# Performance work log

Measured on AMD Instinct MI355X. Metric: run time of the kernel, lower is better.

Reference implementation:

```python
import jax, jax.numpy as jnp
import numpy as np

B, T, D = 4, 2048, 1024


def setup_inputs() -> dict:
    key = jax.random.key(0)
    ks = jax.random.split(key, 7)
    s = 1.0 / np.sqrt(D)
    return {
        "x": jax.random.normal(ks[0], (B, T, D), dtype=jnp.float32),
        "Wq": jax.random.normal(ks[1], (D, D), dtype=jnp.float32) * s,
        "bq": jax.random.normal(ks[2], (D,), dtype=jnp.float32) * s,
        "Wk": jax.random.normal(ks[3], (D, D), dtype=jnp.float32) * s,
        "bk": jax.random.normal(ks[4], (D,), dtype=jnp.float32) * s,
        "Wv": jax.random.normal(ks[5], (D, D), dtype=jnp.float32) * s,
        "bv": jax.random.normal(ks[6], (D,), dtype=jnp.float32) * s,
    }


def reference(x, Wq, bq, Wk, bk, Wv, bv):
    # Linear projections (torch nn.Linear: y = x @ W.T + b)
    Q = jnp.einsum('btd,ed->bte', x, Wq) + bq  # computed for faithfulness; unused downstream
    K = jnp.einsum('btd,ed->bte', x, Wk) + bk
    V = jnp.einsum('btd,ed->bte', x, Wv) + bv
    # Quantum kernel closed form: <ZZ> of RY(a)q0, RY(b)q1, CX(0,1) == cos(b).
    # score[b,i,j] = cos(mean_d K[b,j,d]) -- independent of i (and of Q).
    kmean = K.mean(axis=-1)                      # [B, T]
    scores = jnp.cos(kmean)[:, None, :]          # [B, 1, T] -> broadcast over i
    scores = jax.lax.stop_gradient(jnp.broadcast_to(scores, (Q.shape[0], Q.shape[1], Q.shape[1])))
    weights = jax.nn.softmax(scores, axis=-1)    # [B, T, T]
    return jnp.einsum('bij,bjd->bid', weights, V)
```

## Files before the change

### kernel.cpp

```cpp
#include <hip/hip_runtime.h>

#define D 1024
#define T 2048
#define BATCH 4

typedef float nfloat4 __attribute__((ext_vector_type(4)));

#define WS_WBAR  0
#define WS_BBAR  1024
#define WS_Z     1028
#define WS_ZP    1088
#define WS_U     1664
#define WS_O     5760
#define WS_PART  16384
#define WS_NEED  (((size_t)WS_PART + 4 * 128 * 1024) * 4)

__global__ void __launch_bounds__(256) k_prep(const float4* __restrict__ Wk4,
                                              const float* __restrict__ bk,
                                              float* __restrict__ ws) {
    __shared__ float4 sm[16][17];
    __shared__ float red[256];
    const int bid = blockIdx.x, tid = threadIdx.x;
    if (bid < 16) {
        const int fc = tid & 15, eg = tid >> 4;
        const int d4 = bid * 16 + fc;
        float4 s = make_float4(0.f, 0.f, 0.f, 0.f);
        #pragma unroll 8
        for (int k = 0; k < 64; ++k) {
            const float4 v = Wk4[(eg + k * 16) * 256 + d4];
            s.x += v.x; s.y += v.y; s.z += v.z; s.w += v.w;
        }
        sm[eg][fc] = s;
        __syncthreads();
        if (tid < 16) {
            float4 t = make_float4(0.f, 0.f, 0.f, 0.f);
            #pragma unroll
            for (int g = 0; g < 16; ++g) {
                const float4 v = sm[g][tid];
                t.x += v.x; t.y += v.y; t.z += v.z; t.w += v.w;
            }
            t.x *= (1.0f / D); t.y *= (1.0f / D);
            t.z *= (1.0f / D); t.w *= (1.0f / D);
            ((float4*)(ws + WS_WBAR))[bid * 16 + tid] = t;
        }
    } else if (bid == 16) {
        red[tid] = bk[tid] + bk[tid + 256] + bk[tid + 512] + bk[tid + 768];
        __syncthreads();
        for (int off = 128; off > 0; off >>= 1) {
            if (tid < off) red[tid] += red[tid + off];
            __syncthreads();
        }
        if (tid == 0) ws[WS_BBAR] = red[0] * (1.0f / D);
        if (tid < 4) ws[WS_Z + tid] = 0.f;
    } else {
        float4* u4 = (float4*)(ws + WS_U);
        #pragma unroll
        for (int k = 0; k < 4; ++k)
            u4[k * 256 + tid] = make_float4(0.f, 0.f, 0.f, 0.f);
    }
}

template <bool USE_PART>
__global__ void __launch_bounds__(256) k_pass(const float4* __restrict__ x4,
                                              float* __restrict__ ws) {
    __shared__ float lds[2][4][8];
    const int tid = threadIdx.x, lane = tid & 63, w = tid >> 6;
    const int bid = blockIdx.x;
    const int b = bid >> 7, tc = bid & 127;

    const float4 wq = ((const float4*)(ws + WS_WBAR))[tid];
    const float bbar = ws[WS_BBAR];

    const float4* xr = x4 + (size_t)(b * T + tc * 16) * 256;
    float4 acc = make_float4(0.f, 0.f, 0.f, 0.f);
    float zs = 0.f;

    #pragma unroll
    for (int h = 0; h < 2; ++h) {
        float4 xv[8];
        #pragma unroll
        for (int j = 0; j < 8; ++j) xv[j] = xr[(h * 8 + j) * 256 + tid];
        float p[8];
        #pragma unroll
        for (int j = 0; j < 8; ++j)
            p[j] = xv[j].x * wq.x + xv[j].y * wq.y + xv[j].z * wq.z + xv[j].w * wq.w;
        #pragma unroll
        for (int off = 32; off > 0; off >>= 1) {
            #pragma unroll
            for (int j = 0; j < 8; ++j) p[j] += __shfl_down(p[j], off);
        }
        if (lane == 0) {
            #pragma unroll
            for (int j = 0; j < 8; ++j) lds[h][w][j] = p[j];
        }
        __syncthreads();
        #pragma unroll
        for (int j = 0; j < 8; ++j) {
            const float km = lds[h][0][j] + lds[h][1][j] + lds[h][2][j] + lds[h][3][j] + bbar;
            const float e = expf(cosf(km));
            zs += e;
            acc.x += e * xv[j].x; acc.y += e * xv[j].y;
            acc.z += e * xv[j].z; acc.w += e * xv[j].w;
        }
    }

    if (USE_PART) {
        ((float4*)(ws + WS_PART))[(size_t)bid * 256 + tid] = acc;
        if (tid == 0) ws[WS_ZP + bid] = zs;
    } else {
        float* dst = ws + WS_U + b * D + tid * 4;
        atomicAdd(dst + 0, acc.x);
        atomicAdd(dst + 1, acc.y);
        atomicAdd(dst + 2, acc.z);
        atomicAdd(dst + 3, acc.w);
        if (tid == 0) atomicAdd(ws + WS_Z + b, zs);
    }
}

__global__ void __launch_bounds__(256) k_reduce(float* __restrict__ ws) {
    __shared__ float4 sm[16][17];
    const int bid = blockIdx.x, tid = threadIdx.x;
    const int b = bid >> 4, dc = bid & 15;
    const int dl = tid & 15, pg = tid >> 4;
    const float4* pb = (const float4*)(ws + WS_PART) + (size_t)b * 128 * 256;
    float4 s = make_float4(0.f, 0.f, 0.f, 0.f);
    #pragma unroll
    for (int k = 0; k < 8; ++k) {
        const float4 v = pb[(pg * 8 + k) * 256 + dc * 16 + dl];
        s.x += v.x; s.y += v.y; s.z += v.z; s.w += v.w;
    }
    sm[pg][dl] = s;
    __syncthreads();
    if (tid < 16) {
        float4 t = make_float4(0.f, 0.f, 0.f, 0.f);
        #pragma unroll
        for (int g = 0; g < 16; ++g) {
            const float4 v = sm[g][tid];
            t.x += v.x; t.y += v.y; t.z += v.z; t.w += v.w;
        }
        ((float4*)(ws + WS_U))[b * 256 + dc * 16 + tid] = t;
    }
    if (dc == 0 && tid < 64) {
        float z = ws[WS_ZP + b * 128 + tid] + ws[WS_ZP + b * 128 + 64 + tid];
        #pragma unroll
        for (int off = 32; off > 0; off >>= 1) z += __shfl_down(z, off);
        if (tid == 0) ws[WS_Z + b] = z;
    }
}

__global__ void __launch_bounds__(256) k_proj(const float4* __restrict__ Wv4,
                                              float* __restrict__ ws,
                                              const float* __restrict__ bv) {
    __shared__ float lds[4][4];
    const int tid = threadIdx.x, lane = tid & 63, w = tid >> 6;
    const int d = blockIdx.x;
    const float4 wvv = Wv4[d * 256 + tid];
    const float4* u4 = (const float4*)(ws + WS_U);
    float a[BATCH];
    #pragma unroll
    for (int b = 0; b < BATCH; ++b) {
        const float4 u = u4[b * 256 + tid];
        a[b] = wvv.x * u.x + wvv.y * u.y + wvv.z * u.z + wvv.w * u.w;
    }
    #pragma unroll
    for (int off = 32; off > 0; off >>= 1) {
        #pragma unroll
        for (int b = 0; b < BATCH; ++b) a[b] += __shfl_down(a[b], off);
    }
    if (lane == 0) {
        #pragma unroll
        for (int b = 0; b < BATCH; ++b) lds[w][b] = a[b];
    }
    __syncthreads();
    if (tid == 0) {
        const float bb = bv[d];
        #pragma unroll
        for (int b = 0; b < BATCH; ++b) {
            const float s = lds[0][b] + lds[1][b] + lds[2][b] + lds[3][b];
            ws[WS_O + b * D + d] = s / ws[WS_Z + b] + bb;
        }
    }
}

__global__ void __launch_bounds__(256) k_bcast(const float* __restrict__ ws,
                                               nfloat4* __restrict__ out4) {
    const nfloat4* o4 = (const nfloat4*)(ws + WS_O);
    const int idx = blockIdx.x * 256 + threadIdx.x;
    #pragma unroll
    for (int i = 0; i < 2; ++i) {
        const int f = idx + i * 1048576;
        const nfloat4 v = o4[((f >> 19) << 8) + (f & 255)];
        __builtin_nontemporal_store(v, &out4[f]);
    }
}

extern "C" void kernel_launch(void* const* d_in, const int* in_sizes, int n_in,
                              void* d_out, int out_size, void* d_ws, size_t ws_size,
                              hipStream_t stream) {
    const float* x  = (const float*)d_in[0];
    const float* Wk = (const float*)d_in[3];
    const float* bk = (const float*)d_in[4];
    const float* Wv = (const float*)d_in[5];
    const float* bv = (const float*)d_in[6];
    float* ws  = (float*)d_ws;
    float* out = (float*)d_out;

    const bool use_part = ws_size >= WS_NEED;

    k_prep<<<18, 256, 0, stream>>>((const float4*)Wk, bk, ws);
    if (use_part) {
        k_pass<true><<<512, 256, 0, stream>>>((const float4*)x, ws);
        k_reduce<<<64, 256, 0, stream>>>(ws);
    } else {
        k_pass<false><<<512, 256, 0, stream>>>((const float4*)x, ws);
    }
    k_proj<<<1024, 256, 0, stream>>>((const float4*)Wv, ws, bv);
    k_bcast<<<4096, 256, 0, stream>>>(ws, (nfloat4*)out);
}
```

Before: 33.28 us.

## Drop partial-buffer reduce kernel, always use atomics; load all 16 rows at once

Removes the two-stage reduction path (partial sums written to workspace plus a separate k_reduce launch) and always accumulates per-block results into the output vector with global atomicAdd. This saves one kernel launch and the partial-buffer round trip. In exchange, 512 blocks contend on 4K float atomics, which also makes the summation order nondeterministic. k_pass now loads all 16 rows into registers at once and uses a single barrier instead of two 8-row halves, which raises register pressure.

```diff
diff --git a/kernel.cpp b/kernel.cpp
--- a/kernel.cpp
+++ b/kernel.cpp
@@ -9,11 +9,8 @@
 #define WS_WBAR  0
 #define WS_BBAR  1024
 #define WS_Z     1028
-#define WS_ZP    1088
-#define WS_U     1664
-#define WS_O     5760
-#define WS_PART  16384
-#define WS_NEED  (((size_t)WS_PART + 4 * 128 * 1024) * 4)
+#define WS_U     1536
+#define WS_O     5632
 
 __global__ void __launch_bounds__(256) k_prep(const float4* __restrict__ Wk4,
                                               const float* __restrict__ bk,
@@ -60,10 +57,9 @@
     }
 }
 
-template <bool USE_PART>
 __global__ void __launch_bounds__(256) k_pass(const float4* __restrict__ x4,
                                               float* __restrict__ ws) {
-    __shared__ float lds[2][4][8];
+    __shared__ float lds[4][16];
     const int tid = threadIdx.x, lane = tid & 63, w = tid >> 6;
     const int bid = blockIdx.x;
     const int b = bid >> 7, tc = bid & 127;
@@ -72,80 +68,43 @@
     const float bbar = ws[WS_BBAR];
 
     const float4* xr = x4 + (size_t)(b * T + tc * 16) * 256;
+    float4 xv[16];
+    #pragma unroll
+    for (int j = 0; j < 16; ++j) xv[j] = xr[j * 256 + tid];
+
+    float p[16];
+    #pragma unroll
+    for (int j = 0; j < 16; ++j)
+        p[j] = xv[j].x * wq.x + xv[j].y * wq.y + xv[j].z * wq.z + xv[j].w * wq.w;
+
+    #pragma unroll
+    for (int off = 32; off > 0; off >>= 1) {
+        #pragma unroll
+        for (int j = 0; j < 16; ++j) p[j] += __shfl_down(p[j], off);
+    }
+    if (lane == 0) {
+        #pragma unroll
+        for (int j = 0; j < 16; ++j) lds[w][j] = p[j];
+    }
+    __syncthreads();
+
     float4 acc = make_float4(0.f, 0.f, 0.f, 0.f);
     float zs = 0.f;
-
     #pragma unroll
-    for (int h = 0; h < 2; ++h) {
-        float4 xv[8];
-        #pragma unroll
-        for (int j = 0; j < 8; ++j) xv[j] = xr[(h * 8 + j) * 256 + tid];
-        float p[8];
-        #pragma unroll
-        for (int j = 0; j < 8; ++j)
-            p[j] = xv[j].x * wq.x + xv[j].y * wq.y + xv[j].z * wq.z + xv[j].w * wq.w;
-        #pragma unroll
-        for (int off = 32; off > 0; off >>= 1) {
-            #pragma unroll
-            for (int j = 0; j < 8; ++j) p[j] += __shfl_down(p[j], off);
-        }
-        if (lane == 0) {
-            #pragma unroll
-            for (int j = 0; j < 8; ++j) lds[h][w][j] = p[j];
-        }
-        __syncthreads();
-        #pragma unroll
-        for (int j = 0; j < 8; ++j) {
-            const float km = lds[h][0][j] + lds[h][1][j] + lds[h][2][j] + lds[h][3][j] + bbar;
-            const float e = expf(cosf(km));
-            zs += e;
-            acc.x += e * xv[j].x; acc.y += e * xv[j].y;
-            acc.z += e * xv[j].z; acc.w += e * xv[j].w;
-        }
+    for (int j = 0; j < 16; ++j) {
+        const float km = lds[0][j] + lds[1][j] + lds[2][j] + lds[3][j] + bbar;
+        const float e = expf(cosf(km));
+        zs += e;
+        acc.x += e * xv[j].x; acc.y += e * xv[j].y;
+        acc.z += e * xv[j].z; acc.w += e * xv[j].w;
     }
 
-    if (USE_PART) {
-        ((float4*)(ws + WS_PART))[(size_t)bid * 256 + tid] = acc;
-        if (tid == 0) ws[WS_ZP + bid] = zs;
-    } else {
-        float* dst = ws + WS_U + b * D + tid * 4;
-        atomicAdd(dst + 0, acc.x);
-        atomicAdd(dst + 1, acc.y);
-        atomicAdd(dst + 2, acc.z);
-        atomicAdd(dst + 3, acc.w);
-        if (tid == 0) atomicAdd(ws + WS_Z + b, zs);
-    }
-}
-
-__global__ void __launch_bounds__(256) k_reduce(float* __restrict__ ws) {
-    __shared__ float4 sm[16][17];
-    const int bid = blockIdx.x, tid = threadIdx.x;
-    const int b = bid >> 4, dc = bid & 15;
-    const int dl = tid & 15, pg = tid >> 4;
-    const float4* pb = (const float4*)(ws + WS_PART) + (size_t)b * 128 * 256;
-    float4 s = make_float4(0.f, 0.f, 0.f, 0.f);
-    #pragma unroll
-    for (int k = 0; k < 8; ++k) {
-        const float4 v = pb[(pg * 8 + k) * 256 + dc * 16 + dl];
-        s.x += v.x; s.y += v.y; s.z += v.z; s.w += v.w;
-    }
-    sm[pg][dl] = s;
-    __syncthreads();
-    if (tid < 16) {
-        float4 t = make_float4(0.f, 0.f, 0.f, 0.f);
-        #pragma unroll
-        for (int g = 0; g < 16; ++g) {
-            const float4 v = sm[g][tid];
-            t.x += v.x; t.y += v.y; t.z += v.z; t.w += v.w;
-        }
-        ((float4*)(ws + WS_U))[b * 256 + dc * 16 + tid] = t;
-    }
-    if (dc == 0 && tid < 64) {
-        float z = ws[WS_ZP + b * 128 + tid] + ws[WS_ZP + b * 128 + 64 + tid];
-        #pragma unroll
-        for (int off = 32; off > 0; off >>= 1) z += __shfl_down(z, off);
-        if (tid == 0) ws[WS_Z + b] = z;
-    }
+    float* dst = ws + WS_U + b * D + tid * 4;
+    atomicAdd(dst + 0, acc.x);
+    atomicAdd(dst + 1, acc.y);
+    atomicAdd(dst + 2, acc.z);
+    atomicAdd(dst + 3, acc.w);
+    if (tid == 0) atomicAdd(ws + WS_Z + b, zs);
 }
 
 __global__ void __launch_bounds__(256) k_proj(const float4* __restrict__ Wv4,
@@ -205,15 +164,8 @@
     float* ws  = (float*)d_ws;
     float* out = (float*)d_out;
 
-    const bool use_part = ws_size >= WS_NEED;
-
-    k_prep<<<18, 256, 0, stream>>>((const float4*)Wk, bk, ws);
-    if (use_part) {
-        k_pass<true><<<512, 256, 0, stream>>>((const float4*)x, ws);
-        k_reduce<<<64, 256, 0, stream>>>(ws);
-    } else {
-        k_pass<false><<<512, 256, 0, stream>>>((const float4*)x, ws);
-    }
-    k_proj<<<1024, 256, 0, stream>>>((const float4*)Wv, ws, bv);
+    k_prep <<<18, 256, 0, stream>>>((const float4*)Wk, bk, ws);
+    k_pass <<<512, 256, 0, stream>>>((const float4*)x, ws);
+    k_proj <<<1024, 256, 0, stream>>>((const float4*)Wv, ws, bv);
     k_bcast<<<4096, 256, 0, stream>>>(ws, (nfloat4*)out);
 }
```

Measured after the change: 47.10 us. 41.5% more time.
